# Kernel optimization log

Measured on AMD Instinct MI355X. Metric: run time of the kernel, lower is better.

## Reference

```python
import jax, jax.numpy as jnp
import numpy as np

D_MODEL = 2048
NUM_HEADS = 32
NUM_KV_GROUPS = 8
D_K = D_MODEL // NUM_HEADS  # 64
KV_DIM = D_K * NUM_KV_GROUPS  # 512
B, S = 2, 2048


def setup_inputs() -> dict:
    key = jax.random.key(0)
    ks = jax.random.split(key, 9)
    sd = 1.0 / np.sqrt(D_MODEL).astype(np.float32)
    return {
        "x": jax.random.normal(ks[0], (B, S, D_MODEL), jnp.float32),
        "wq": jax.random.normal(ks[1], (D_MODEL, D_MODEL), jnp.float32) * sd,
        "bq": jnp.zeros((D_MODEL,), jnp.float32),
        "wk": jax.random.normal(ks[2], (D_MODEL, KV_DIM), jnp.float32) * sd,
        "bk": jnp.zeros((KV_DIM,), jnp.float32),
        "wv": jax.random.normal(ks[3], (D_MODEL, KV_DIM), jnp.float32) * sd,
        "bv": jnp.zeros((KV_DIM,), jnp.float32),
        "wo": jax.random.normal(ks[4], (D_MODEL, D_MODEL), jnp.float32) * sd,
        "bo": jnp.zeros((D_MODEL,), jnp.float32),
    }


def reference(x, wq, bq, wk, bk, wv, bv, wo, bo):
    b, s, _ = x.shape
    # projections (torch Linear = x @ W^T + b; weights here stored as (in,out))
    Q = (x @ wq + bq).reshape(b, s, NUM_HEADS, D_K).transpose(0, 2, 1, 3)       # [B,H,S,dk]
    K = (x @ wk + bk).reshape(b, s, NUM_KV_GROUPS, D_K).transpose(0, 2, 1, 3)   # [B,G,S,dk]
    V = (x @ wv + bv).reshape(b, s, NUM_KV_GROUPS, D_K).transpose(0, 2, 1, 3)   # [B,G,S,dk]
    kv_repeat = NUM_HEADS // NUM_KV_GROUPS
    K_rep = jnp.repeat(K, kv_repeat, axis=1)  # [B,H,S,dk]
    V_rep = jnp.repeat(V, kv_repeat, axis=1)  # [B,H,S,dk]
    scale = 1.0 / jnp.sqrt(jnp.asarray(D_K, x.dtype))
    attn_scores = jnp.einsum("bhqd,bhkd->bhqk", Q, K_rep) * scale
    attn_weights = jax.nn.softmax(attn_scores, axis=-1)                          # [B,H,S,S]
    context = jnp.einsum("bhqk,bhkd->bhqd", attn_weights, V_rep)
    context = context.transpose(0, 2, 1, 3).reshape(b, s, D_MODEL)
    return context @ wo + bo
```

## Files before the change

### kernel.cpp

```cpp
#include <hip/hip_runtime.h>
#include <hip/hip_bf16.h>

typedef __bf16 v8bf16 __attribute__((ext_vector_type(8)));
typedef __bf16 bf16x4 __attribute__((ext_vector_type(4)));
typedef float  f32x4  __attribute__((ext_vector_type(4)));

#define D_MODEL 2048
#define S_LEN   2048
#define NHEADS  32
#define NGROUPS 8
#define DK      64
#define NTOK    4096
#define NQKV    3072
#define QSCALE  0.18033688011112042f

__device__ __forceinline__ void lds_load16(const void* g, void* l) {
  __builtin_amdgcn_global_load_lds(
      (__attribute__((address_space(1))) unsigned int*)g,
      (__attribute__((address_space(3))) unsigned int*)l, 16, 0, 0);
}

__global__ __launch_bounds__(256)
void cvt_f32_bf16(const float* __restrict__ in, __bf16* __restrict__ out, int n) {
  int i = (blockIdx.x * 256 + threadIdx.x) * 4;
  if (i >= n) return;
  float4 v = *(const float4*)(in + i);
  bf16x4 o = { (__bf16)v.x, (__bf16)v.y, (__bf16)v.z, (__bf16)v.w };
  *(bf16x4*)(out + i) = o;
}

__global__ __launch_bounds__(256)
void transpose_cvt(const float* __restrict__ in, __bf16* __restrict__ out, int R, int C) {
  __shared__ float tile[32][33];
  int tx = threadIdx.x, ty = threadIdx.y;
  int c0 = blockIdx.x * 32, r0 = blockIdx.y * 32;
#pragma unroll
  for (int j = 0; j < 4; j++)
    tile[ty + 8 * j][tx] = in[(size_t)(r0 + ty + 8 * j) * C + c0 + tx];
  __syncthreads();
#pragma unroll
  for (int j = 0; j < 4; j++)
    out[(size_t)(c0 + ty + 8 * j) * R + r0 + tx] = (__bf16)tile[tx][ty + 8 * j];
}

__global__ __launch_bounds__(256)
void transpose_bf16(const __bf16* __restrict__ in, __bf16* __restrict__ out,
                    int R, int C, int ldin, int ldout) {
  __shared__ __bf16 tile[32][33];
  int tx = threadIdx.x, ty = threadIdx.y;
  int c0 = blockIdx.x * 32, r0 = blockIdx.y * 32;
#pragma unroll
  for (int j = 0; j < 4; j++)
    tile[ty + 8 * j][tx] = in[(size_t)(r0 + ty + 8 * j) * ldin + c0 + tx];
  __syncthreads();
#pragma unroll
  for (int j = 0; j < 4; j++)
    out[(size_t)(c0 + ty + 8 * j) * ldout + r0 + tx] = tile[tx][ty + 8 * j];
}

template <int MODE>
__global__ __launch_bounds__(256, 2)
void gemm_bt(const __bf16* __restrict__ A, const __bf16* __restrict__ BT,
             const float* __restrict__ b0, const float* __restrict__ b1,
             const float* __restrict__ b2,
             __bf16* __restrict__ Cb, float* __restrict__ Cf,
             int M, int N, int K) {
  __shared__ __bf16 As[128 * 32];
  __shared__ __bf16 Bs[128 * 32];
  const int t = threadIdx.x;
  const int lane = t & 63, w = t >> 6;
  const int lr = lane & 15, lg = lane >> 4;
  const int gx = gridDim.x;
  const int flat = blockIdx.y * gx + blockIdx.x;
  const int cpx = (gx * gridDim.y) >> 3;
  const int sb = (flat & 7) * cpx + (flat >> 3);
  const int m0 = (sb / gx) * 128, n0 = (sb % gx) * 128;
  const int rm = (w >> 1) * 64, cn = (w & 1) * 64;
  const int srow = t >> 2, scol = (t & 3) * 8;

  const f32x4 fz = {0.f, 0.f, 0.f, 0.f};
  f32x4 acc[4][4];
#pragma unroll
  for (int mi = 0; mi < 4; mi++)
#pragma unroll
    for (int ni = 0; ni < 4; ni++) acc[mi][ni] = fz;

  for (int kt = 0; kt < K; kt += 32) {
    __syncthreads();
    lds_load16(A + (size_t)(m0 + srow) * K + kt + scol, As + w * 512);
    lds_load16(A + (size_t)(m0 + 64 + srow) * K + kt + scol, As + 2048 + w * 512);
    lds_load16(BT + (size_t)(n0 + srow) * K + kt + scol, Bs + w * 512);
    lds_load16(BT + (size_t)(n0 + 64 + srow) * K + kt + scol, Bs + 2048 + w * 512);
    __syncthreads();
    v8bf16 af[4], bfr[4];
#pragma unroll
    for (int i = 0; i < 4; i++)
      af[i] = *(const v8bf16*)&As[(rm + i * 16 + lr) * 32 + lg * 8];
#pragma unroll
    for (int i = 0; i < 4; i++)
      bfr[i] = *(const v8bf16*)&Bs[(cn + i * 16 + lr) * 32 + lg * 8];
#pragma unroll
    for (int mi = 0; mi < 4; mi++)
#pragma unroll
      for (int ni = 0; ni < 4; ni++)
        acc[mi][ni] = __builtin_amdgcn_mfma_f32_16x16x32_bf16(af[mi], bfr[ni], acc[mi][ni], 0, 0, 0);
  }

#pragma unroll
  for (int ni = 0; ni < 4; ni++) {
    int col = n0 + cn + ni * 16 + lr;
    float bias, scale = 1.0f;
    if (MODE == 0) {
      if (col < 2048)      { bias = b0[col];        scale = QSCALE; }
      else if (col < 2560) { bias = b1[col - 2048]; }
      else                 { bias = b2[col - 2560]; }
    } else {
      bias = b0[col];
    }
#pragma unroll
    for (int mi = 0; mi < 4; mi++)
#pragma unroll
      for (int r = 0; r < 4; r++) {
        int row = m0 + rm + mi * 16 + lg * 4 + r;
        float v = acc[mi][ni][r] + bias;
        if (MODE == 0) Cb[(size_t)row * N + col] = (__bf16)(v * scale);
        else           Cf[(size_t)row * N + col] = v;
      }
  }
}

__global__ __launch_bounds__(512, 2)
void attn_kernel(const __bf16* __restrict__ QKV, const __bf16* __restrict__ VT,
                 __bf16* __restrict__ ctx) {
  __shared__ __bf16 smem[26624];
  const int t = threadIdx.x;
  const int lane = t & 63, w = t >> 6;
  const int lr = lane & 15, lg = lane >> 4;
  const int flat = blockIdx.y * 8 + blockIdx.x;
  const int swz = (flat & 7) * 64 + (flat >> 3);
  const int qt = swz & 7, bh = swz >> 3;
  const int b = bh >> 5, h = bh & 31, g = h >> 2;
  const int q0 = qt * 256;
  const int scol = (((t & 7) ^ ((t >> 3) & 7)) << 3);

  v8bf16 qa[2][2];
#pragma unroll
  for (int mi = 0; mi < 2; mi++)
#pragma unroll
    for (int dk2 = 0; dk2 < 2; dk2++)
      qa[mi][dk2] = *(const v8bf16*)(QKV +
          (size_t)(b * S_LEN + q0 + w * 32 + mi * 16 + lr) * NQKV + h * DK + dk2 * 32 + lg * 8);

  const __bf16* kp = QKV + (size_t)(b * S_LEN + (t >> 3)) * NQKV + D_MODEL + g * DK + scol;
  const __bf16* vp = VT + (size_t)(g * DK + (t >> 3)) * NTOK + b * S_LEN + scol;

  lds_load16(kp, smem + t * 8);
  lds_load16(vp, smem + 4096 + t * 8);
  __syncthreads();

  const int kloff0 = lr * 64 + ((lg * 8) ^ ((lr & 7) << 3));
  const int kloff1 = lr * 64 + ((32 + lg * 8) ^ ((lr & 7) << 3));
  __bf16* Pw = smem + 16384 + w * 1280;

  const __bf16 one1 = (__bf16)1.0f;
  const v8bf16 ones = { one1, one1, one1, one1, one1, one1, one1, one1 };
  const f32x4 fz = {0.f, 0.f, 0.f, 0.f};
  f32x4 o[2][4], o_sum[2];
  o_sum[0] = fz; o_sum[1] = fz;
#pragma unroll
  for (int mi = 0; mi < 2; mi++)
#pragma unroll
    for (int nd = 0; nd < 4; nd++) o[mi][nd] = fz;

#pragma unroll 2
  for (int kt = 0; kt < 32; kt++) {
    if (kt < 31) {
      __bf16* nb = smem + ((kt & 1) ^ 1) * 8192;
      lds_load16(kp + (size_t)64 * NQKV, nb + t * 8);
      lds_load16(vp + 64, nb + 4096 + t * 8);
      kp += (size_t)64 * NQKV;
      vp += 64;
    }
    const __bf16* Kb = smem + (kt & 1) * 8192;
    const __bf16* k0 = Kb + kloff0;
    const __bf16* k1 = Kb + kloff1;

    f32x4 st[4][2];
#pragma unroll
    for (int ni = 0; ni < 4; ni++) { st[ni][0] = fz; st[ni][1] = fz; }
    __builtin_amdgcn_s_setprio(1);
#pragma unroll
    for (int ni = 0; ni < 4; ni++) {
      v8bf16 kb = *(const v8bf16*)(k0 + ni * 1024);
      st[ni][0] = __builtin_amdgcn_mfma_f32_16x16x32_bf16(kb, qa[0][0], st[ni][0], 0, 0, 0);
      st[ni][1] = __builtin_amdgcn_mfma_f32_16x16x32_bf16(kb, qa[1][0], st[ni][1], 0, 0, 0);
    }
#pragma unroll
    for (int ni = 0; ni < 4; ni++) {
      v8bf16 kb = *(const v8bf16*)(k1 + ni * 1024);
      st[ni][0] = __builtin_amdgcn_mfma_f32_16x16x32_bf16(kb, qa[0][1], st[ni][0], 0, 0, 0);
      st[ni][1] = __builtin_amdgcn_mfma_f32_16x16x32_bf16(kb, qa[1][1], st[ni][1], 0, 0, 0);
    }
    __builtin_amdgcn_s_setprio(0);

#pragma unroll
    for (int ks = 0; ks < 2; ks++) {
      const __bf16* vbase = (ks ? k1 : k0) + 4096;
#pragma unroll
      for (int mi = 0; mi < 2; mi++)
#pragma unroll
        for (int ni2 = 0; ni2 < 2; ni2++) {
          f32x4 sv = st[2 * ks + ni2][mi];
          bf16x4 pk = { (__bf16)exp2f(sv[0]), (__bf16)exp2f(sv[1]),
                        (__bf16)exp2f(sv[2]), (__bf16)exp2f(sv[3]) };
          *(bf16x4*)(Pw + (mi * 16 + lr) * 40 + ni2 * 16 + lg * 4) = pk;
        }
      v8bf16 pa0 = *(const v8bf16*)(Pw + lr * 40 + lg * 8);
      v8bf16 pa1 = *(const v8bf16*)(Pw + (16 + lr) * 40 + lg * 8);
      __builtin_amdgcn_s_setprio(1);
#pragma unroll
      for (int nd = 0; nd < 4; nd++) {
        v8bf16 vb = *(const v8bf16*)(vbase + nd * 1024);
        o[0][nd] = __builtin_amdgcn_mfma_f32_16x16x32_bf16(pa0, vb, o[0][nd], 0, 0, 0);
        o[1][nd] = __builtin_amdgcn_mfma_f32_16x16x32_bf16(pa1, vb, o[1][nd], 0, 0, 0);
      }
      o_sum[0] = __builtin_amdgcn_mfma_f32_16x16x32_bf16(pa0, ones, o_sum[0], 0, 0, 0);
      o_sum[1] = __builtin_amdgcn_mfma_f32_16x16x32_bf16(pa1, ones, o_sum[1], 0, 0, 0);
      __builtin_amdgcn_s_setprio(0);
    }

    __syncthreads();
  }

#pragma unroll
  for (int mi = 0; mi < 2; mi++)
#pragma unroll
    for (int r = 0; r < 4; r++) {
      float inv = 1.0f / o_sum[mi][r];
      int row = b * S_LEN + q0 + w * 32 + mi * 16 + lg * 4 + r;
#pragma unroll
      for (int nd = 0; nd < 4; nd++)
        ctx[(size_t)row * D_MODEL + h * DK + nd * 16 + lr] = (__bf16)(o[mi][nd][r] * inv);
    }
}

extern "C" void kernel_launch(void* const* d_in, const int* in_sizes, int n_in,
                              void* d_out, int out_size, void* d_ws, size_t ws_size,
                              hipStream_t stream) {
  (void)in_sizes; (void)n_in; (void)out_size; (void)ws_size;
  const float* x  = (const float*)d_in[0];
  const float* wq = (const float*)d_in[1];
  const float* bq = (const float*)d_in[2];
  const float* wk = (const float*)d_in[3];
  const float* bk = (const float*)d_in[4];
  const float* wv = (const float*)d_in[5];
  const float* bv = (const float*)d_in[6];
  const float* wo = (const float*)d_in[7];
  const float* bo = (const float*)d_in[8];

  char* ws = (char*)d_ws;
  __bf16* xb    = (__bf16*)(ws);
  __bf16* wqkvT = (__bf16*)(ws + 16777216);
  __bf16* woT   = (__bf16*)(ws + 29360128);
  __bf16* QKVb  = (__bf16*)(ws + 37748736);
  __bf16* VbT   = (__bf16*)(ws + 62914560);
  __bf16* ctx   = (__bf16*)(ws + 67108864);

  dim3 tb(32, 8);
  cvt_f32_bf16<<<8192, 256, 0, stream>>>(x, xb, NTOK * D_MODEL);
  transpose_cvt<<<dim3(64, 64), tb, 0, stream>>>(wq, wqkvT, 2048, 2048);
  transpose_cvt<<<dim3(16, 64), tb, 0, stream>>>(wk, wqkvT + 2048 * 2048, 2048, 512);
  transpose_cvt<<<dim3(16, 64), tb, 0, stream>>>(wv, wqkvT + 2560 * 2048, 2048, 512);
  transpose_cvt<<<dim3(64, 64), tb, 0, stream>>>(wo, woT, 2048, 2048);

  gemm_bt<0><<<dim3(24, 32), 256, 0, stream>>>(xb, wqkvT, bq, bk, bv,
                                               QKVb, nullptr, NTOK, NQKV, 2048);
  transpose_bf16<<<dim3(16, 128), tb, 0, stream>>>(QKVb + 2560, VbT, 4096, 512, 3072, 4096);
  attn_kernel<<<dim3(8, 64), 512, 0, stream>>>(QKVb, VbT, ctx);
  gemm_bt<1><<<dim3(16, 32), 256, 0, stream>>>(ctx, woT, bo, nullptr, nullptr,
                                               nullptr, (float*)d_out, NTOK, 2048, 2048);
}
```

Baseline: 228.2 us.

## Triple-buffer K/V tiles in attention with one barrier per iteration

Replaces the double-buffered K/V staging loop in the attention kernel with a three-buffer ring. Loads run two tiles ahead, and each iteration uses a partial vmcnt wait plus a single barrier instead of a full syncthreads at the end. The goal is to hide global-to-LDS load latency behind the MFMA work and cut the synchronisation stall. In exchange, LDS use per block grows, which could lower occupancy, and the hand-written waitcnt accounting has to stay correct.

Result: no change. 229.9 us (+0.7%).

```diff
diff --git a/kernel.cpp b/kernel.cpp
--- a/kernel.cpp
+++ b/kernel.cpp
@@ -132,7 +132,7 @@
 __global__ __launch_bounds__(512, 2)
 void attn_kernel(const __bf16* __restrict__ QKV, const __bf16* __restrict__ VT,
                  __bf16* __restrict__ ctx) {
-  __shared__ __bf16 smem[26624];
+  __shared__ __bf16 smem[34816];
   const int t = threadIdx.x;
   const int lane = t & 63, w = t >> 6;
   const int lr = lane & 15, lg = lane >> 4;
@@ -154,13 +154,23 @@
   const __bf16* kp = QKV + (size_t)(b * S_LEN + (t >> 3)) * NQKV + D_MODEL + g * DK + scol;
   const __bf16* vp = VT + (size_t)(g * DK + (t >> 3)) * NTOK + b * S_LEN + scol;
 
-  lds_load16(kp, smem + t * 8);
-  lds_load16(vp, smem + 4096 + t * 8);
-  __syncthreads();
+  auto stage = [&](__bf16* buf) {
+    lds_load16(kp, buf + t * 8);
+    lds_load16(vp, buf + 4096 + t * 8);
+    kp += (size_t)64 * NQKV;
+    vp += 64;
+  };
+
+  __bf16* bufA = smem;
+  __bf16* bufB = smem + 8192;
+  __bf16* bufC = smem + 16384;
+
+  stage(bufA);
+  stage(bufB);
 
   const int kloff0 = lr * 64 + ((lg * 8) ^ ((lr & 7) << 3));
   const int kloff1 = lr * 64 + ((32 + lg * 8) ^ ((lr & 7) << 3));
-  __bf16* Pw = smem + 16384 + w * 1280;
+  __bf16* Pw = smem + 24576 + w * 1280;
 
   const __bf16 one1 = (__bf16)1.0f;
   const v8bf16 ones = { one1, one1, one1, one1, one1, one1, one1, one1 };
@@ -172,19 +182,9 @@
 #pragma unroll
     for (int nd = 0; nd < 4; nd++) o[mi][nd] = fz;
 
-#pragma unroll 2
-  for (int kt = 0; kt < 32; kt++) {
-    if (kt < 31) {
-      __bf16* nb = smem + ((kt & 1) ^ 1) * 8192;
-      lds_load16(kp + (size_t)64 * NQKV, nb + t * 8);
-      lds_load16(vp + 64, nb + 4096 + t * 8);
-      kp += (size_t)64 * NQKV;
-      vp += 64;
-    }
-    const __bf16* Kb = smem + (kt & 1) * 8192;
+  auto compute = [&](const __bf16* Kb) {
     const __bf16* k0 = Kb + kloff0;
     const __bf16* k1 = Kb + kloff1;
-
     f32x4 st[4][2];
 #pragma unroll
     for (int ni = 0; ni < 4; ni++) { st[ni][0] = fz; st[ni][1] = fz; }
@@ -228,9 +228,23 @@
       o_sum[1] = __builtin_amdgcn_mfma_f32_16x16x32_bf16(pa1, ones, o_sum[1], 0, 0, 0);
       __builtin_amdgcn_s_setprio(0);
     }
-
-    __syncthreads();
+  };
+
+  __bf16* cur = bufA;
+  __bf16* nxt = bufB;
+  __bf16* fre = bufC;
+  for (int kt = 0; kt < 31; kt++) {
+    asm volatile("s_waitcnt vmcnt(2)" ::: "memory");
+    __builtin_amdgcn_s_barrier();
+    __builtin_amdgcn_sched_barrier(0);
+    if (kt < 30) stage(fre);
+    compute(cur);
+    __bf16* tmp = cur; cur = nxt; nxt = fre; fre = tmp;
   }
+  asm volatile("s_waitcnt vmcnt(0)" ::: "memory");
+  __builtin_amdgcn_s_barrier();
+  __builtin_amdgcn_sched_barrier(0);
+  compute(cur);
 
 #pragma unroll
   for (int mi = 0; mi < 2; mi++)
```

## Halve attention query tile to 16 rows per wave and raise occupancy

Applied to the files above, without the earlier changes.

Each wave in the attention kernel now handles 16 query rows instead of 32, so a block covers 128 queries and the grid doubles to 1024 blocks. Launch bounds rise from 2 to 6 blocks per CU, and the shared memory for P shrinks, cutting register and LDS pressure. The cost is twice as many K/V tile loads into LDS in total and less reuse of each loaded K/V fragment across MFMAs.

Result: slower. 233.8 us (+2.4%).

```diff
diff --git a/kernel.cpp b/kernel.cpp
--- a/kernel.cpp
+++ b/kernel.cpp
@@ -129,27 +129,25 @@
   }
 }
 
-__global__ __launch_bounds__(512, 2)
+__global__ __launch_bounds__(512, 6)
 void attn_kernel(const __bf16* __restrict__ QKV, const __bf16* __restrict__ VT,
                  __bf16* __restrict__ ctx) {
-  __shared__ __bf16 smem[26624];
+  __shared__ __bf16 smem[21504];
   const int t = threadIdx.x;
   const int lane = t & 63, w = t >> 6;
   const int lr = lane & 15, lg = lane >> 4;
-  const int flat = blockIdx.y * 8 + blockIdx.x;
-  const int swz = (flat & 7) * 64 + (flat >> 3);
-  const int qt = swz & 7, bh = swz >> 3;
+  const int flat = blockIdx.y * 16 + blockIdx.x;
+  const int swz = (flat & 7) * 128 + (flat >> 3);
+  const int qt = swz & 15, bh = swz >> 4;
   const int b = bh >> 5, h = bh & 31, g = h >> 2;
-  const int q0 = qt * 256;
+  const int q0 = qt * 128;
   const int scol = (((t & 7) ^ ((t >> 3) & 7)) << 3);
 
-  v8bf16 qa[2][2];
-#pragma unroll
-  for (int mi = 0; mi < 2; mi++)
-#pragma unroll
-    for (int dk2 = 0; dk2 < 2; dk2++)
-      qa[mi][dk2] = *(const v8bf16*)(QKV +
-          (size_t)(b * S_LEN + q0 + w * 32 + mi * 16 + lr) * NQKV + h * DK + dk2 * 32 + lg * 8);
+  v8bf16 qa[2];
+#pragma unroll
+  for (int dk2 = 0; dk2 < 2; dk2++)
+    qa[dk2] = *(const v8bf16*)(QKV +
+        (size_t)(b * S_LEN + q0 + w * 16 + lr) * NQKV + h * DK + dk2 * 32 + lg * 8);
 
   const __bf16* kp = QKV + (size_t)(b * S_LEN + (t >> 3)) * NQKV + D_MODEL + g * DK + scol;
   const __bf16* vp = VT + (size_t)(g * DK + (t >> 3)) * NTOK + b * S_LEN + scol;
@@ -160,17 +158,15 @@
 
   const int kloff0 = lr * 64 + ((lg * 8) ^ ((lr & 7) << 3));
   const int kloff1 = lr * 64 + ((32 + lg * 8) ^ ((lr & 7) << 3));
-  __bf16* Pw = smem + 16384 + w * 1280;
+  __bf16* Pw = smem + 16384 + w * 640;
 
   const __bf16 one1 = (__bf16)1.0f;
   const v8bf16 ones = { one1, one1, one1, one1, one1, one1, one1, one1 };
   const f32x4 fz = {0.f, 0.f, 0.f, 0.f};
-  f32x4 o[2][4], o_sum[2];
-  o_sum[0] = fz; o_sum[1] = fz;
-#pragma unroll
-  for (int mi = 0; mi < 2; mi++)
-#pragma unroll
-    for (int nd = 0; nd < 4; nd++) o[mi][nd] = fz;
+  f32x4 o[4], o_sum;
+  o_sum = fz;
+#pragma unroll
+  for (int nd = 0; nd < 4; nd++) o[nd] = fz;
 
 #pragma unroll 2
   for (int kt = 0; kt < 32; kt++) {
@@ -185,21 +181,19 @@
     const __bf16* k0 = Kb + kloff0;
     const __bf16* k1 = Kb + kloff1;
 
-    f32x4 st[4][2];
-#pragma unroll
-    for (int ni = 0; ni < 4; ni++) { st[ni][0] = fz; st[ni][1] = fz; }
+    f32x4 st[4];
+#pragma unroll
+    for (int ni = 0; ni < 4; ni++) st[ni] = fz;
     __builtin_amdgcn_s_setprio(1);
 #pragma unroll
     for (int ni = 0; ni < 4; ni++) {
       v8bf16 kb = *(const v8bf16*)(k0 + ni * 1024);
-      st[ni][0] = __builtin_amdgcn_mfma_f32_16x16x32_bf16(kb, qa[0][0], st[ni][0], 0, 0, 0);
-      st[ni][1] = __builtin_amdgcn_mfma_f32_16x16x32_bf16(kb, qa[1][0], st[ni][1], 0, 0, 0);
+      st[ni] = __builtin_amdgcn_mfma_f32_16x16x32_bf16(kb, qa[0], st[ni], 0, 0, 0);
     }
 #pragma unroll
     for (int ni = 0; ni < 4; ni++) {
       v8bf16 kb = *(const v8bf16*)(k1 + ni * 1024);
-      st[ni][0] = __builtin_amdgcn_mfma_f32_16x16x32_bf16(kb, qa[0][1], st[ni][0], 0, 0, 0);
-      st[ni][1] = __builtin_amdgcn_mfma_f32_16x16x32_bf16(kb, qa[1][1], st[ni][1], 0, 0, 0);
+      st[ni] = __builtin_amdgcn_mfma_f32_16x16x32_bf16(kb, qa[1], st[ni], 0, 0, 0);
     }
     __builtin_amdgcn_s_setprio(0);
 
@@ -207,25 +201,20 @@
     for (int ks = 0; ks < 2; ks++) {
       const __bf16* vbase = (ks ? k1 : k0) + 4096;
 #pragma unroll
-      for (int mi = 0; mi < 2; mi++)
-#pragma unroll
-        for (int ni2 = 0; ni2 < 2; ni2++) {
-          f32x4 sv = st[2 * ks + ni2][mi];
-          bf16x4 pk = { (__bf16)exp2f(sv[0]), (__bf16)exp2f(sv[1]),
-                        (__bf16)exp2f(sv[2]), (__bf16)exp2f(sv[3]) };
-          *(bf16x4*)(Pw + (mi * 16 + lr) * 40 + ni2 * 16 + lg * 4) = pk;
-        }
-      v8bf16 pa0 = *(const v8bf16*)(Pw + lr * 40 + lg * 8);
-      v8bf16 pa1 = *(const v8bf16*)(Pw + (16 + lr) * 40 + lg * 8);
+      for (int ni2 = 0; ni2 < 2; ni2++) {
+        f32x4 sv = st[2 * ks + ni2];
+        bf16x4 pk = { (__bf16)exp2f(sv[0]), (__bf16)exp2f(sv[1]),
+                      (__bf16)exp2f(sv[2]), (__bf16)exp2f(sv[3]) };
+        *(bf16x4*)(Pw + lr * 40 + ni2 * 16 + lg * 4) = pk;
+      }
+      v8bf16 pa = *(const v8bf16*)(Pw + lr * 40 + lg * 8);
       __builtin_amdgcn_s_setprio(1);
 #pragma unroll
       for (int nd = 0; nd < 4; nd++) {
         v8bf16 vb = *(const v8bf16*)(vbase + nd * 1024);
-        o[0][nd] = __builtin_amdgcn_mfma_f32_16x16x32_bf16(pa0, vb, o[0][nd], 0, 0, 0);
-        o[1][nd] = __builtin_amdgcn_mfma_f32_16x16x32_bf16(pa1, vb, o[1][nd], 0, 0, 0);
+        o[nd] = __builtin_amdgcn_mfma_f32_16x16x32_bf16(pa, vb, o[nd], 0, 0, 0);
       }
-      o_sum[0] = __builtin_amdgcn_mfma_f32_16x16x32_bf16(pa0, ones, o_sum[0], 0, 0, 0);
-      o_sum[1] = __builtin_amdgcn_mfma_f32_16x16x32_bf16(pa1, ones, o_sum[1], 0, 0, 0);
+      o_sum = __builtin_amdgcn_mfma_f32_16x16x32_bf16(pa, ones, o_sum, 0, 0, 0);
       __builtin_amdgcn_s_setprio(0);
     }
 
@@ -233,15 +222,13 @@
   }
 
 #pragma unroll
-  for (int mi = 0; mi < 2; mi++)
-#pragma unroll
-    for (int r = 0; r < 4; r++) {
-      float inv = 1.0f / o_sum[mi][r];
-      int row = b * S_LEN + q0 + w * 32 + mi * 16 + lg * 4 + r;
-#pragma unroll
-      for (int nd = 0; nd < 4; nd++)
-        ctx[(size_t)row * D_MODEL + h * DK + nd * 16 + lr] = (__bf16)(o[mi][nd][r] * inv);
-    }
+  for (int r = 0; r < 4; r++) {
+    float inv = 1.0f / o_sum[r];
+    int row = b * S_LEN + q0 + w * 16 + lg * 4 + r;
+#pragma unroll
+    for (int nd = 0; nd < 4; nd++)
+      ctx[(size_t)row * D_MODEL + h * DK + nd * 16 + lr] = (__bf16)(o[nd][r] * inv);
+  }
 }
 
 extern "C" void kernel_launch(void* const* d_in, const int* in_sizes, int n_in,
@@ -276,7 +263,7 @@
   gemm_bt<0><<<dim3(24, 32), 256, 0, stream>>>(xb, wqkvT, bq, bk, bv,
                                                QKVb, nullptr, NTOK, NQKV, 2048);
   transpose_bf16<<<dim3(16, 128), tb, 0, stream>>>(QKVb + 2560, VbT, 4096, 512, 3072, 4096);
-  attn_kernel<<<dim3(8, 64), 512, 0, stream>>>(QKVb, VbT, ctx);
+  attn_kernel<<<dim3(16, 64), 512, 0, stream>>>(QKVb, VbT, ctx);
   gemm_bt<1><<<dim3(16, 32), 256, 0, stream>>>(ctx, woT, bo, nullptr, nullptr,
                                                nullptr, (float*)d_out, NTOK, 2048, 2048);
 }
```

## Replace GEMMs with double-buffered large-tile kernel using swizzled LDS

Applied to the files above, without the earlier changes.

Replaces the 128x128, K=32, single-buffered GEMM with a 512-thread kernel that uses 256xBN tiles and K=64 steps. Global-to-LDS loads are double-buffered with explicit vmcnt waits so the next tile loads while the current one computes. An XOR swizzle on LDS columns avoids bank conflicts, and s_setprio raises priority around the MFMA bursts. Grids shrink to 256 blocks, one wave of work on the chip. In exchange the kernel uses more registers and LDS, and it hard-codes K=2048 and the vmcnt counts.

Measured after the change: 231.1 us. No clear change (+1.2%).

```diff
diff --git a/kernel.cpp b/kernel.cpp
--- a/kernel.cpp
+++ b/kernel.cpp
@@ -20,6 +20,10 @@
       (__attribute__((address_space(3))) unsigned int*)l, 16, 0, 0);
 }
 
+__device__ __forceinline__ int sw64(int row, int col) {
+  return row * 64 + (col ^ ((row & 7) << 3));
+}
+
 __global__ __launch_bounds__(256)
 void cvt_f32_bf16(const float* __restrict__ in, __bf16* __restrict__ out, int n) {
   int i = (blockIdx.x * 256 + threadIdx.x) * 4;
@@ -58,57 +62,90 @@
     out[(size_t)(c0 + ty + 8 * j) * ldout + r0 + tx] = tile[tx][ty + 8 * j];
 }
 
-template <int MODE>
-__global__ __launch_bounds__(256, 2)
-void gemm_bt(const __bf16* __restrict__ A, const __bf16* __restrict__ BT,
-             const float* __restrict__ b0, const float* __restrict__ b1,
-             const float* __restrict__ b2,
-             __bf16* __restrict__ Cb, float* __restrict__ Cf,
-             int M, int N, int K) {
-  __shared__ __bf16 As[128 * 32];
-  __shared__ __bf16 Bs[128 * 32];
+template <int MODE, int BN>
+__global__ __launch_bounds__(512, 1)
+void gemm_big(const __bf16* __restrict__ A, const __bf16* __restrict__ BT,
+              const float* __restrict__ b0, const float* __restrict__ b1,
+              const float* __restrict__ b2,
+              __bf16* __restrict__ Cb, float* __restrict__ Cf,
+              int M, int N, int K) {
+  constexpr int FN = BN / 64;
+  __shared__ __bf16 Alds[2 * 256 * 64];
+  __shared__ __bf16 Blds[2 * BN * 64];
   const int t = threadIdx.x;
   const int lane = t & 63, w = t >> 6;
   const int lr = lane & 15, lg = lane >> 4;
-  const int gx = gridDim.x;
-  const int flat = blockIdx.y * gx + blockIdx.x;
-  const int cpx = (gx * gridDim.y) >> 3;
-  const int sb = (flat & 7) * cpx + (flat >> 3);
-  const int m0 = (sb / gx) * 128, n0 = (sb % gx) * 128;
-  const int rm = (w >> 1) * 64, cn = (w & 1) * 64;
-  const int srow = t >> 2, scol = (t & 3) * 8;
+  const int wm = w >> 2, wn = w & 3;
+  const int cpx = gridDim.x >> 3;
+  const int swz = (blockIdx.x & 7) * cpx + (blockIdx.x >> 3);
+  const int nbx = N / BN;
+  const int m0 = (swz / nbx) * 256, n0 = (swz % nbx) * BN;
+  const int scol = (((t & 7) ^ ((t >> 3) & 7)) << 3);
+
+  const __bf16* ap = A + (size_t)(m0 + (t >> 3)) * K + scol;
+  const __bf16* bp = BT + (size_t)(n0 + (t >> 3)) * K + scol;
+
+  auto stage = [&](int buf) {
+    __bf16* ad = Alds + buf * 16384 + t * 8;
+    __bf16* bd = Blds + buf * BN * 64 + t * 8;
+#pragma unroll
+    for (int i = 0; i < 4; i++) lds_load16(ap + (size_t)i * 64 * K, ad + i * 4096);
+#pragma unroll
+    for (int i = 0; i < FN; i++) lds_load16(bp + (size_t)i * 64 * K, bd + i * 4096);
+    ap += 64; bp += 64;
+  };
 
   const f32x4 fz = {0.f, 0.f, 0.f, 0.f};
-  f32x4 acc[4][4];
-#pragma unroll
-  for (int mi = 0; mi < 4; mi++)
-#pragma unroll
-    for (int ni = 0; ni < 4; ni++) acc[mi][ni] = fz;
-
-  for (int kt = 0; kt < K; kt += 32) {
-    __syncthreads();
-    lds_load16(A + (size_t)(m0 + srow) * K + kt + scol, As + w * 512);
-    lds_load16(A + (size_t)(m0 + 64 + srow) * K + kt + scol, As + 2048 + w * 512);
-    lds_load16(BT + (size_t)(n0 + srow) * K + kt + scol, Bs + w * 512);
-    lds_load16(BT + (size_t)(n0 + 64 + srow) * K + kt + scol, Bs + 2048 + w * 512);
-    __syncthreads();
-    v8bf16 af[4], bfr[4];
-#pragma unroll
-    for (int i = 0; i < 4; i++)
-      af[i] = *(const v8bf16*)&As[(rm + i * 16 + lr) * 32 + lg * 8];
-#pragma unroll
-    for (int i = 0; i < 4; i++)
-      bfr[i] = *(const v8bf16*)&Bs[(cn + i * 16 + lr) * 32 + lg * 8];
-#pragma unroll
-    for (int mi = 0; mi < 4; mi++)
-#pragma unroll
-      for (int ni = 0; ni < 4; ni++)
-        acc[mi][ni] = __builtin_amdgcn_mfma_f32_16x16x32_bf16(af[mi], bfr[ni], acc[mi][ni], 0, 0, 0);
+  f32x4 acc[8][FN];
+#pragma unroll
+  for (int fm = 0; fm < 8; fm++)
+#pragma unroll
+    for (int fn = 0; fn < FN; fn++) acc[fm][fn] = fz;
+
+  auto compute = [&](int buf) {
+    const __bf16* Ab = Alds + buf * 16384;
+    const __bf16* Bb = Blds + buf * BN * 64;
+#pragma unroll
+    for (int ks = 0; ks < 2; ks++) {
+      v8bf16 bfr[FN];
+#pragma unroll
+      for (int fn = 0; fn < FN; fn++)
+        bfr[fn] = *(const v8bf16*)&Bb[sw64(wn * (BN / 4) + fn * 16 + lr, ks * 32 + lg * 8)];
+      __builtin_amdgcn_s_setprio(1);
+#pragma unroll
+      for (int fm = 0; fm < 8; fm++) {
+        v8bf16 af = *(const v8bf16*)&Ab[sw64(wm * 128 + fm * 16 + lr, ks * 32 + lg * 8)];
+#pragma unroll
+        for (int fn = 0; fn < FN; fn++)
+          acc[fm][fn] = __builtin_amdgcn_mfma_f32_16x16x32_bf16(af, bfr[fn], acc[fm][fn], 0, 0, 0);
+      }
+      __builtin_amdgcn_s_setprio(0);
+    }
+  };
+
+  stage(0);
+  stage(1);
+  for (int kt = 0; kt < 32; kt++) {
+    if (kt < 31) {
+      if constexpr (FN == 3) asm volatile("s_waitcnt vmcnt(7)" ::: "memory");
+      else                   asm volatile("s_waitcnt vmcnt(6)" ::: "memory");
+    } else {
+      asm volatile("s_waitcnt vmcnt(0)" ::: "memory");
+    }
+    __builtin_amdgcn_s_barrier();
+    __builtin_amdgcn_sched_barrier(0);
+    compute(kt & 1);
+    if (kt < 30) {
+      __builtin_amdgcn_sched_barrier(0);
+      __builtin_amdgcn_s_barrier();
+      __builtin_amdgcn_sched_barrier(0);
+      stage(kt & 1);
+    }
   }
 
 #pragma unroll
-  for (int ni = 0; ni < 4; ni++) {
-    int col = n0 + cn + ni * 16 + lr;
+  for (int fn = 0; fn < FN; fn++) {
+    int col = n0 + wn * (BN / 4) + fn * 16 + lr;
     float bias, scale = 1.0f;
     if (MODE == 0) {
       if (col < 2048)      { bias = b0[col];        scale = QSCALE; }
@@ -118,11 +155,11 @@
       bias = b0[col];
     }
 #pragma unroll
-    for (int mi = 0; mi < 4; mi++)
+    for (int fm = 0; fm < 8; fm++)
 #pragma unroll
       for (int r = 0; r < 4; r++) {
-        int row = m0 + rm + mi * 16 + lg * 4 + r;
-        float v = acc[mi][ni][r] + bias;
+        int row = m0 + wm * 128 + fm * 16 + lg * 4 + r;
+        float v = acc[fm][fn][r] + bias;
         if (MODE == 0) Cb[(size_t)row * N + col] = (__bf16)(v * scale);
         else           Cf[(size_t)row * N + col] = v;
       }
@@ -273,10 +310,10 @@
   transpose_cvt<<<dim3(16, 64), tb, 0, stream>>>(wv, wqkvT + 2560 * 2048, 2048, 512);
   transpose_cvt<<<dim3(64, 64), tb, 0, stream>>>(wo, woT, 2048, 2048);
 
-  gemm_bt<0><<<dim3(24, 32), 256, 0, stream>>>(xb, wqkvT, bq, bk, bv,
-                                               QKVb, nullptr, NTOK, NQKV, 2048);
+  gemm_big<0, 192><<<dim3(256), 512, 0, stream>>>(xb, wqkvT, bq, bk, bv,
+                                                  QKVb, nullptr, NTOK, NQKV, 2048);
   transpose_bf16<<<dim3(16, 128), tb, 0, stream>>>(QKVb + 2560, VbT, 4096, 512, 3072, 4096);
   attn_kernel<<<dim3(8, 64), 512, 0, stream>>>(QKVb, VbT, ctx);
-  gemm_bt<1><<<dim3(16, 32), 256, 0, stream>>>(ctx, woT, bo, nullptr, nullptr,
-                                               nullptr, (float*)d_out, NTOK, 2048, 2048);
-}
+  gemm_big<1, 128><<<dim3(256), 512, 0, stream>>>(ctx, woT, bo, nullptr, nullptr,
+                                                  nullptr, (float*)d_out, NTOK, 2048, 2048);
+}
```
